# Performance work log

Hardware: AMD Instinct MI355X
Metric: run time of the kernel (lower is better)

Reference implementation:

```python
import jax, jax.numpy as jnp
import numpy as np

B, LQ, LA, H = 32, 1024, 1024, 512
NEG = -1e7


def setup_inputs() -> dict:
    key = jax.random.key(0)
    kq, ka, ku = jax.random.split(key, 3)
    q = jax.random.normal(kq, (B, LQ, H), dtype=jnp.float32)
    a = jax.random.normal(ka, (B, LA, H), dtype=jnp.float32)
    U = 0.02 * jax.random.normal(ku, (H, H), dtype=jnp.float32)  # init.normal(std=0.02)
    q_mask = jnp.ones((B, LQ, 1), dtype=jnp.float32)
    a_mask = jnp.ones((B, LA, 1), dtype=jnp.float32)
    return {"q": q, "a": a, "U": U, "q_mask": q_mask, "a_mask": a_mask}


def reference(q, a, U, q_mask, a_mask):
    # mask[b,i,j] = q_mask[b,i] * a_mask[b,j]  (nonzero => valid)
    mask = jnp.matmul(q_mask, jnp.swapaxes(a_mask, 1, 2)) > 0  # [B,LQ,LA] bool
    # bilinear score X = q @ U @ a^T
    qU = jnp.einsum('bqh,hk->bqk', q, U)
    X = jnp.einsum('bqk,bak->bqa', qU, a)  # [B,LQ,LA]
    X = jnp.where(mask, X, NEG)
    I = jax.nn.sigmoid(X)
    att_a2q = jnp.max(jax.nn.softmax(I, axis=-1), axis=-1)  # [B,LQ]
    att_q2a = jnp.max(jax.nn.softmax(I, axis=-2), axis=-2)  # [B,LA]
    q_attn = jnp.einsum('blh,bl->bh', q, att_a2q)  # [B,H]
    a_attn = jnp.einsum('blh,bl->bh', a, att_q2a)  # [B,H]
    return q_attn, a_attn
```

## Files before the change

kernel.cpp:

```cpp
#include <hip/hip_runtime.h>

typedef __attribute__((ext_vector_type(8))) short bf16x8;
typedef __attribute__((ext_vector_type(4))) float f32x4;
typedef unsigned short u16;
typedef unsigned int u32;

#define NLOG2E -1.44269504088896f
#define LOG2E   1.44269504088896f

__device__ __forceinline__ float bf2f(u16 x) {
  union { u32 u; float f; } v; v.u = ((u32)x) << 16; return v.f;
}
__device__ __forceinline__ u16 f2b(float f) {
  union { float f; u32 u; } v; v.f = f;
  return (u16)((v.u + 0x7FFFu + ((v.u >> 16) & 1u)) >> 16);
}
__device__ __forceinline__ bool inputs_are_bf16(const void* qmask) {
  return *(const u32*)qmask == 0x3F803F80u;
}
__device__ __forceinline__ u32 fkey(float f) {
  u32 b = __float_as_uint(f);
  return (b >> 31) ? ~b : (b | 0x80000000u);
}
__device__ __forceinline__ float fkey_inv(u32 k) {
  u32 b = (k & 0x80000000u) ? (k ^ 0x80000000u) : ~k;
  return __uint_as_float(b);
}

__global__ __launch_bounds__(256) void prep_all(
    const void* __restrict__ q, const void* __restrict__ a,
    const void* __restrict__ U, const void* __restrict__ qmask,
    u16* __restrict__ qb, u16* __restrict__ ab, u16* __restrict__ Ut,
    u32* __restrict__ stats, float* __restrict__ out)
{
  const bool bf = inputs_are_bf16(qmask);
  const int t = threadIdx.x;
  __shared__ u16 tile[64][65];
  if (blockIdx.x < 8192) {
    const int idx = blockIdx.x * 256 + t;
    if (idx < 131072) stats[idx] = (idx < 65536) ? 0u : 0xFFFFFFFFu;
    if (idx < 32768) out[idx] = 0.f;
    const size_t base = (size_t)idx * 8;
    if (bf) {
      *(bf16x8*)&qb[base] = ((const bf16x8*)q)[idx];
      *(bf16x8*)&ab[base] = ((const bf16x8*)a)[idx];
    } else {
      const float4* qf = (const float4*)q;
      const float4* af = (const float4*)a;
      float4 x0 = qf[2 * idx], x1 = qf[2 * idx + 1];
      u16 o[8] = {f2b(x0.x), f2b(x0.y), f2b(x0.z), f2b(x0.w),
                  f2b(x1.x), f2b(x1.y), f2b(x1.z), f2b(x1.w)};
      *(bf16x8*)&qb[base] = *(bf16x8*)o;
      float4 y0 = af[2 * idx], y1 = af[2 * idx + 1];
      u16 p[8] = {f2b(y0.x), f2b(y0.y), f2b(y0.z), f2b(y0.w),
                  f2b(y1.x), f2b(y1.y), f2b(y1.z), f2b(y1.w)};
      *(bf16x8*)&ab[base] = *(bf16x8*)p;
    }
  } else {
    const int bb = blockIdx.x - 8192;
    const int bx = bb & 7, by = bb >> 3;
    #pragma unroll
    for (int i = 0; i < 16; i++) {
      int r = i * 4 + (t >> 6);
      int c = t & 63;
      size_t gi = (size_t)(by * 64 + r) * 512 + bx * 64 + c;
      tile[c][r] = bf ? ((const u16*)U)[gi] : f2b(((const float*)U)[gi]);
    }
    __syncthreads();
    #pragma unroll
    for (int i = 0; i < 16; i++) {
      int r = i * 4 + (t >> 6);
      int c = t & 63;
      Ut[(size_t)(bx * 64 + r) * 512 + by * 64 + c] = tile[r][c];
    }
  }
}

template<int EPI>
__global__ __launch_bounds__(256) void gemm_bt(
    const u16* __restrict__ A, const u16* __restrict__ B,
    u16* __restrict__ C, float scaleC,
    size_t strideA, size_t strideB,
    const void* __restrict__ q_mask, const void* __restrict__ a_mask,
    float* __restrict__ rowsumA, float* __restrict__ colsumA,
    u32* __restrict__ rowkeyA, u32* __restrict__ colkeyA)
{
  __shared__ __align__(16) char smem[37888];
  u16* As = (u16*)smem;
  u16* Bs = (u16*)(smem + 16384);
  u16* Ct = (u16*)smem;
  float* redS = (float*)smem;
  float* redM = (float*)(smem + 16896);
  float* qp = (float*)(smem + 36864);
  float* ap = (float*)(smem + 37376);

  int bx, by, bz;
  if (EPI) {
    const int id = blockIdx.x;
    bz = id >> 6;
    const int w = id & 63;
    bx = w >> 3;
    by = ((w & 7) - bz) & 7;
  } else {
    bx = blockIdx.x; by = blockIdx.y; bz = blockIdx.z;
  }

  const int tid  = threadIdx.x;
  const int lane = tid & 63;
  const int wave = tid >> 6;
  const int wr = wave >> 1, wc = wave & 1;
  const int l15 = lane & 15, lq = lane >> 4;
  const int rsub = lane >> 3;
  const int csw  = (lane & 7) ^ rsub;

  const u16* Ab = A + strideA * bz + (size_t)by * 128 * 512;
  const u16* Bb = B + strideB * bz + (size_t)bx * 128 * 512;

  if (EPI) {
    const bool bf = inputs_are_bf16(q_mask);
    if (tid < 128) {
      int gi = bz * 1024 + by * 128 + tid;
      float v = bf ? bf2f(((const u16*)q_mask)[gi]) : ((const float*)q_mask)[gi];
      qp[tid] = (v > 0.f) ? 0.f : 1e30f;
    } else {
      int gj = bz * 1024 + bx * 128 + (tid - 128);
      float v = bf ? bf2f(((const u16*)a_mask)[gj]) : ((const float*)a_mask)[gj];
      ap[tid - 128] = (v > 0.f) ? 0.f : 1e30f;
    }
    __syncthreads();
  }

  f32x4 acc[4][4];
  if (EPI) {
    #pragma unroll
    for (int mt = 0; mt < 4; mt++)
      #pragma unroll
      for (int nt = 0; nt < 4; nt++) {
        float cp = ap[wc * 64 + nt * 16 + l15];
        #pragma unroll
        for (int r = 0; r < 4; r++)
          acc[mt][nt][r] = qp[wr * 64 + mt * 16 + lq * 4 + r] + cp;
      }
  } else {
    #pragma unroll
    for (int i = 0; i < 4; i++)
      #pragma unroll
      for (int j = 0; j < 4; j++) {
        f32x4 z = {0.f, 0.f, 0.f, 0.f};
        acc[i][j] = z;
      }
  }

  for (int k0 = 0; k0 < 512; k0 += 64) {
    #pragma unroll
    for (int i = 0; i < 4; i++) {
      const int r0 = wave * 32 + i * 8;
      const size_t go = (size_t)(r0 + rsub) * 512 + k0 + csw * 8;
      __builtin_amdgcn_global_load_lds(
          (const __attribute__((address_space(1))) void*)(Ab + go),
          (__attribute__((address_space(3))) void*)&As[r0 * 64], 16, 0, 0);
      __builtin_amdgcn_global_load_lds(
          (const __attribute__((address_space(1))) void*)(Bb + go),
          (__attribute__((address_space(3))) void*)&Bs[r0 * 64], 16, 0, 0);
    }
    __syncthreads();
    #pragma unroll
    for (int ks = 0; ks < 64; ks += 32) {
      const int cx = ((ks >> 3) + lq) ^ (l15 & 7);
      bf16x8 af[4], bfr[4];
      #pragma unroll
      for (int tt = 0; tt < 4; tt++) {
        af[tt]  = *(const bf16x8*)&As[(wr * 64 + tt * 16 + l15) * 64 + cx * 8];
        bfr[tt] = *(const bf16x8*)&Bs[(wc * 64 + tt * 16 + l15) * 64 + cx * 8];
      }
      #pragma unroll
      for (int mt = 0; mt < 4; mt++)
        #pragma unroll
        for (int nt = 0; nt < 4; nt++)
          acc[mt][nt] = __builtin_amdgcn_mfma_f32_16x16x32_bf16(af[mt], bfr[nt], acc[mt][nt], 0, 0, 0);
    }
    __syncthreads();
  }

  if (!EPI) {
    #pragma unroll
    for (int mt = 0; mt < 4; mt++)
      #pragma unroll
      for (int nt = 0; nt < 4; nt++)
        #pragma unroll
        for (int r = 0; r < 4; r++) {
          int row = wr * 64 + mt * 16 + lq * 4 + r;
          int col = wc * 64 + nt * 16 + l15;
          Ct[row * 144 + col] = f2b(scaleC * acc[mt][nt][r]);
        }
    __syncthreads();
    u16* Cb = C + (size_t)by * 128 * 512 + bx * 128;
    #pragma unroll
    for (int i = 0; i < 8; i++) {
      int c = tid + i * 256;
      int row = c >> 4, cc = c & 15;
      *(bf16x8*)&Cb[(size_t)row * 512 + cc * 8] = *(const bf16x8*)&Ct[row * 144 + cc * 8];
    }
  } else {
    const int gi0 = bz * 1024 + by * 128;
    const int gj0 = bz * 1024 + bx * 128;
    float csum[4] = {0.f, 0.f, 0.f, 0.f};
    float cmin[4] = {3e38f, 3e38f, 3e38f, 3e38f};
    #pragma unroll
    for (int mt = 0; mt < 4; mt++) {
      #pragma unroll
      for (int r = 0; r < 4; r++) {
        const int row = wr * 64 + mt * 16 + lq * 4 + r;
        float rsm = 0.f, rmn = 3e38f;
        #pragma unroll
        for (int nt = 0; nt < 4; nt++) {
          float y = acc[mt][nt][r];
          float u = __builtin_amdgcn_exp2f(y);
          float s = __builtin_amdgcn_rcpf(1.f + u);
          float e = __builtin_amdgcn_exp2f(LOG2E * s);
          rsm += e;
          csum[nt] += e;
          rmn = fminf(rmn, y);
          cmin[nt] = fminf(cmin[nt], y);
        }
        redS[row * 33 + l15 + 16 * wc] = rsm;
        redM[row * 33 + l15 + 16 * wc] = rmn;
      }
    }
    #pragma unroll
    for (int nt = 0; nt < 4; nt++) {
      float cs = csum[nt], cm = cmin[nt];
      cs += __shfl_xor(cs, 16); cm = fminf(cm, __shfl_xor(cm, 16));
      cs += __shfl_xor(cs, 32); cm = fminf(cm, __shfl_xor(cm, 32));
      if (lane < 16) {
        int gj = gj0 + wc * 64 + nt * 16 + l15;
        atomicAdd(&colsumA[gj], cs);
        atomicMin(&colkeyA[gj], fkey(cm));
      }
    }
    __syncthreads();
    if (tid < 128) {
      float s = 0.f;
      #pragma unroll
      for (int j = 0; j < 32; j++) s += redS[tid * 33 + j];
      atomicAdd(&rowsumA[gi0 + tid], s);
    } else {
      const int row = tid - 128;
      float m = 3e38f;
      #pragma unroll
      for (int j = 0; j < 32; j++) m = fminf(m, redM[row * 33 + j]);
      atomicMin(&rowkeyA[gi0 + row], fkey(m));
    }
  }
}

__global__ __launch_bounds__(256) void partial_kernel(
    const u16* __restrict__ qb, const u16* __restrict__ ab,
    const u32* __restrict__ stats, float* __restrict__ out)
{
  __shared__ float att[128];
  const int tid = threadIdx.x;
  const int hc = blockIdx.x, seg = blockIdx.y;
  const int b = blockIdx.z >> 1, half = blockIdx.z & 1;
  const float* sm = (const float*)stats + half * 32768 + b * 1024 + seg * 128;
  const u32* ky = stats + 65536 + half * 32768 + b * 1024 + seg * 128;
  if (tid < 128) {
    float ymin = fkey_inv(ky[tid]);
    float Imax = __builtin_amdgcn_rcpf(1.f + __builtin_amdgcn_exp2f(ymin));
    att[tid] = __expf(Imax) * __builtin_amdgcn_rcpf(sm[tid]);
  }
  __syncthreads();
  const u16* src = (half ? ab : qb) + (size_t)b * 524288 + (size_t)seg * 128 * 512;
  const int h = hc * 256 + tid;
  float acc = 0.f;
  #pragma unroll 8
  for (int i = 0; i < 128; i++) acc += bf2f(src[(size_t)i * 512 + h]) * att[i];
  atomicAdd(&out[half * 16384 + b * 512 + h], acc);
}

extern "C" void kernel_launch(void* const* d_in, const int* in_sizes, int n_in,
                              void* d_out, int out_size, void* d_ws, size_t ws_size,
                              hipStream_t stream) {
  const void* q  = d_in[0];
  const void* a  = d_in[1];
  const void* U  = d_in[2];
  const void* qm = d_in[3];
  const void* am = d_in[4];
  float* out = (float*)d_out;

  char* ws = (char*)d_ws;
  u16* qb    = (u16*)ws;
  u16* ab    = (u16*)(ws + 33554432);
  u16* qU    = (u16*)(ws + 67108864);
  u16* Ut    = (u16*)(ws + 100663296);
  u32* stats = (u32*)(ws + 101187584);
  float* rowsumA = (float*)stats;
  float* colsumA = (float*)stats + 32768;
  u32* rowkeyA = stats + 65536;
  u32* colkeyA = stats + 98304;

  prep_all<<<dim3(8256), dim3(256), 0, stream>>>(q, a, U, qm, qb, ab, Ut, stats, out);
  gemm_bt<0><<<dim3(4, 256, 1), dim3(256), 0, stream>>>(
      qb, Ut, qU, NLOG2E, (size_t)0, (size_t)0, qm, am,
      rowsumA, colsumA, rowkeyA, colkeyA);
  gemm_bt<1><<<dim3(2048), dim3(256), 0, stream>>>(
      qU, ab, (u16*)nullptr, 1.f, (size_t)524288, (size_t)524288, qm, am,
      rowsumA, colsumA, rowkeyA, colkeyA);
  partial_kernel<<<dim3(2, 8, 64), dim3(256), 0, stream>>>(qb, ab, stats, out);
}
```

Measured before the change: 257.9 us.

## Double-buffer GEMM LDS staging and replace stat atomics with per-slice partials

Both GEMM kernels now prefetch the next K-tile into a second LDS buffer while computing the current one. They use explicit vmcnt waits and barriers instead of two __syncthreads per iteration, and declare launch bounds for two blocks per CU. The score GEMM no longer does float atomicAdd and key-encoded atomicMin into global row and column stats. It writes per-tile partial sums and minima into slices, and partial_kernel reduces them, which also removes the stats init from prep_all. The costs are a larger LDS footprint, a plain 3D grid instead of the old swizzled block order, and reuse of the Ut workspace region for the partials once the first GEMM has finished.

```diff
diff --git a/kernel.cpp b/kernel.cpp
--- a/kernel.cpp
+++ b/kernel.cpp
@@ -7,6 +7,7 @@
 
 #define NLOG2E -1.44269504088896f
 #define LOG2E   1.44269504088896f
+#define SLICE 32768
 
 __device__ __forceinline__ float bf2f(u16 x) {
   union { u32 u; float f; } v; v.u = ((u32)x) << 16; return v.f;
@@ -17,28 +18,19 @@
 }
 __device__ __forceinline__ bool inputs_are_bf16(const void* qmask) {
   return *(const u32*)qmask == 0x3F803F80u;
-}
-__device__ __forceinline__ u32 fkey(float f) {
-  u32 b = __float_as_uint(f);
-  return (b >> 31) ? ~b : (b | 0x80000000u);
-}
-__device__ __forceinline__ float fkey_inv(u32 k) {
-  u32 b = (k & 0x80000000u) ? (k ^ 0x80000000u) : ~k;
-  return __uint_as_float(b);
 }
 
 __global__ __launch_bounds__(256) void prep_all(
     const void* __restrict__ q, const void* __restrict__ a,
     const void* __restrict__ U, const void* __restrict__ qmask,
     u16* __restrict__ qb, u16* __restrict__ ab, u16* __restrict__ Ut,
-    u32* __restrict__ stats, float* __restrict__ out)
+    float* __restrict__ out)
 {
   const bool bf = inputs_are_bf16(qmask);
   const int t = threadIdx.x;
   __shared__ u16 tile[64][65];
   if (blockIdx.x < 8192) {
     const int idx = blockIdx.x * 256 + t;
-    if (idx < 131072) stats[idx] = (idx < 65536) ? 0u : 0xFFFFFFFFu;
     if (idx < 32768) out[idx] = 0.f;
     const size_t base = (size_t)idx * 8;
     if (bf) {
@@ -77,34 +69,27 @@
 }
 
 template<int EPI>
-__global__ __launch_bounds__(256) void gemm_bt(
+__global__ __launch_bounds__(256, 2) void gemm_bt(
     const u16* __restrict__ A, const u16* __restrict__ B,
     u16* __restrict__ C, float scaleC,
     size_t strideA, size_t strideB,
     const void* __restrict__ q_mask, const void* __restrict__ a_mask,
-    float* __restrict__ rowsumA, float* __restrict__ colsumA,
-    u32* __restrict__ rowkeyA, u32* __restrict__ colkeyA)
+    float* __restrict__ statsP)
 {
-  __shared__ __align__(16) char smem[37888];
-  u16* As = (u16*)smem;
-  u16* Bs = (u16*)(smem + 16384);
-  u16* Ct = (u16*)smem;
+  __shared__ __align__(16) char smem[66560];
+  u16* As0 = (u16*)smem;
+  u16* Bs0 = (u16*)(smem + 16384);
+  u16* As1 = (u16*)(smem + 32768);
+  u16* Bs1 = (u16*)(smem + 49152);
+  u16* Ct  = (u16*)smem;
   float* redS = (float*)smem;
   float* redM = (float*)(smem + 16896);
-  float* qp = (float*)(smem + 36864);
-  float* ap = (float*)(smem + 37376);
-
-  int bx, by, bz;
-  if (EPI) {
-    const int id = blockIdx.x;
-    bz = id >> 6;
-    const int w = id & 63;
-    bx = w >> 3;
-    by = ((w & 7) - bz) & 7;
-  } else {
-    bx = blockIdx.x; by = blockIdx.y; bz = blockIdx.z;
-  }
-
+  float* colS = (float*)(smem + 33792);
+  float* colM = (float*)(smem + 34816);
+  float* qp = (float*)(smem + 65536);
+  float* ap = (float*)(smem + 66048);
+
+  const int bx = blockIdx.x, by = blockIdx.y, bz = blockIdx.z;
   const int tid  = threadIdx.x;
   const int lane = tid & 63;
   const int wave = tid >> 6;
@@ -151,27 +136,39 @@
       }
   }
 
-  for (int k0 = 0; k0 < 512; k0 += 64) {
+  auto stage = [&](u16* Asb, u16* Bsb, int k0) {
     #pragma unroll
     for (int i = 0; i < 4; i++) {
       const int r0 = wave * 32 + i * 8;
       const size_t go = (size_t)(r0 + rsub) * 512 + k0 + csw * 8;
       __builtin_amdgcn_global_load_lds(
           (const __attribute__((address_space(1))) void*)(Ab + go),
-          (__attribute__((address_space(3))) void*)&As[r0 * 64], 16, 0, 0);
+          (__attribute__((address_space(3))) void*)&Asb[r0 * 64], 16, 0, 0);
       __builtin_amdgcn_global_load_lds(
           (const __attribute__((address_space(1))) void*)(Bb + go),
-          (__attribute__((address_space(3))) void*)&Bs[r0 * 64], 16, 0, 0);
-    }
-    __syncthreads();
+          (__attribute__((address_space(3))) void*)&Bsb[r0 * 64], 16, 0, 0);
+    }
+  };
+
+  stage(As0, Bs0, 0);
+  #pragma unroll
+  for (int t = 0; t < 8; t++) {
+    u16* Asc = (t & 1) ? As1 : As0;
+    u16* Bsc = (t & 1) ? Bs1 : Bs0;
+    if (t < 7) {
+      stage((t & 1) ? As0 : As1, (t & 1) ? Bs0 : Bs1, (t + 1) * 64);
+      asm volatile("s_waitcnt vmcnt(8)\n\ts_barrier" ::: "memory");
+    } else {
+      asm volatile("s_waitcnt vmcnt(0)\n\ts_barrier" ::: "memory");
+    }
     #pragma unroll
     for (int ks = 0; ks < 64; ks += 32) {
       const int cx = ((ks >> 3) + lq) ^ (l15 & 7);
       bf16x8 af[4], bfr[4];
       #pragma unroll
       for (int tt = 0; tt < 4; tt++) {
-        af[tt]  = *(const bf16x8*)&As[(wr * 64 + tt * 16 + l15) * 64 + cx * 8];
-        bfr[tt] = *(const bf16x8*)&Bs[(wc * 64 + tt * 16 + l15) * 64 + cx * 8];
+        af[tt]  = *(const bf16x8*)&Asc[(wr * 64 + tt * 16 + l15) * 64 + cx * 8];
+        bfr[tt] = *(const bf16x8*)&Bsc[(wc * 64 + tt * 16 + l15) * 64 + cx * 8];
       }
       #pragma unroll
       for (int mt = 0; mt < 4; mt++)
@@ -179,7 +176,7 @@
         for (int nt = 0; nt < 4; nt++)
           acc[mt][nt] = __builtin_amdgcn_mfma_f32_16x16x32_bf16(af[mt], bfr[nt], acc[mt][nt], 0, 0, 0);
     }
-    __syncthreads();
+    asm volatile("s_waitcnt lgkmcnt(0)\n\ts_barrier" ::: "memory");
   }
 
   if (!EPI) {
@@ -204,6 +201,11 @@
   } else {
     const int gi0 = bz * 1024 + by * 128;
     const int gj0 = bz * 1024 + bx * 128;
+    float* rowsumP = statsP + 0      + bx * SLICE;
+    float* colsumP = statsP + 262144 + by * SLICE;
+    float* rowminP = statsP + 524288 + bx * SLICE;
+    float* colminP = statsP + 786432 + by * SLICE;
+
     float csum[4] = {0.f, 0.f, 0.f, 0.f};
     float cmin[4] = {3e38f, 3e38f, 3e38f, 3e38f};
     #pragma unroll
@@ -233,9 +235,9 @@
       cs += __shfl_xor(cs, 16); cm = fminf(cm, __shfl_xor(cm, 16));
       cs += __shfl_xor(cs, 32); cm = fminf(cm, __shfl_xor(cm, 32));
       if (lane < 16) {
-        int gj = gj0 + wc * 64 + nt * 16 + l15;
-        atomicAdd(&colsumA[gj], cs);
-        atomicMin(&colkeyA[gj], fkey(cm));
+        int j = wc * 64 + nt * 16 + l15;
+        colS[j * 2 + wr] = cs;
+        colM[j * 2 + wr] = cm;
       }
     }
     __syncthreads();
@@ -243,31 +245,39 @@
       float s = 0.f;
       #pragma unroll
       for (int j = 0; j < 32; j++) s += redS[tid * 33 + j];
-      atomicAdd(&rowsumA[gi0 + tid], s);
+      rowsumP[gi0 + tid] = s;
+      colsumP[gj0 + tid] = colS[tid * 2] + colS[tid * 2 + 1];
     } else {
-      const int row = tid - 128;
+      const int r = tid - 128;
       float m = 3e38f;
       #pragma unroll
-      for (int j = 0; j < 32; j++) m = fminf(m, redM[row * 33 + j]);
-      atomicMin(&rowkeyA[gi0 + row], fkey(m));
+      for (int j = 0; j < 32; j++) m = fminf(m, redM[r * 33 + j]);
+      rowminP[gi0 + r] = m;
+      colminP[gj0 + r] = fminf(colM[r * 2], colM[r * 2 + 1]);
     }
   }
 }
 
 __global__ __launch_bounds__(256) void partial_kernel(
     const u16* __restrict__ qb, const u16* __restrict__ ab,
-    const u32* __restrict__ stats, float* __restrict__ out)
+    const float* __restrict__ statsP, float* __restrict__ out)
 {
   __shared__ float att[128];
   const int tid = threadIdx.x;
   const int hc = blockIdx.x, seg = blockIdx.y;
   const int b = blockIdx.z >> 1, half = blockIdx.z & 1;
-  const float* sm = (const float*)stats + half * 32768 + b * 1024 + seg * 128;
-  const u32* ky = stats + 65536 + half * 32768 + b * 1024 + seg * 128;
   if (tid < 128) {
-    float ymin = fkey_inv(ky[tid]);
-    float Imax = __builtin_amdgcn_rcpf(1.f + __builtin_amdgcn_exp2f(ymin));
-    att[tid] = __expf(Imax) * __builtin_amdgcn_rcpf(sm[tid]);
+    const int g = b * 1024 + seg * 128 + tid;
+    const float* sumP = statsP + half * 262144;
+    const float* minP = statsP + 524288 + half * 262144;
+    float s = 0.f, m = 3e38f;
+    #pragma unroll
+    for (int s8 = 0; s8 < 8; s8++) {
+      s += sumP[s8 * SLICE + g];
+      m = fminf(m, minP[s8 * SLICE + g]);
+    }
+    float Imax = __builtin_amdgcn_rcpf(1.f + __builtin_amdgcn_exp2f(m));
+    att[tid] = __expf(Imax) * __builtin_amdgcn_rcpf(s);
   }
   __syncthreads();
   const u16* src = (half ? ab : qb) + (size_t)b * 524288 + (size_t)seg * 128 * 512;
@@ -293,18 +303,12 @@
   u16* ab    = (u16*)(ws + 33554432);
   u16* qU    = (u16*)(ws + 67108864);
   u16* Ut    = (u16*)(ws + 100663296);
-  u32* stats = (u32*)(ws + 101187584);
-  float* rowsumA = (float*)stats;
-  float* colsumA = (float*)stats + 32768;
-  u32* rowkeyA = stats + 65536;
-  u32* colkeyA = stats + 98304;
-
-  prep_all<<<dim3(8256), dim3(256), 0, stream>>>(q, a, U, qm, qb, ab, Ut, stats, out);
+  float* statsP = (float*)(ws + 100663296);
+
+  prep_all<<<dim3(8256), dim3(256), 0, stream>>>(q, a, U, qm, qb, ab, Ut, out);
   gemm_bt<0><<<dim3(4, 256, 1), dim3(256), 0, stream>>>(
-      qb, Ut, qU, NLOG2E, (size_t)0, (size_t)0, qm, am,
-      rowsumA, colsumA, rowkeyA, colkeyA);
-  gemm_bt<1><<<dim3(2048), dim3(256), 0, stream>>>(
-      qU, ab, (u16*)nullptr, 1.f, (size_t)524288, (size_t)524288, qm, am,
-      rowsumA, colsumA, rowkeyA, colkeyA);
-  partial_kernel<<<dim3(2, 8, 64), dim3(256), 0, stream>>>(qb, ab, stats, out);
-}
+      qb, Ut, qU, NLOG2E, (size_t)0, (size_t)0, qm, am, statsP);
+  gemm_bt<1><<<dim3(8, 8, 32), dim3(256), 0, stream>>>(
+      qU, ab, (u16*)nullptr, 1.f, (size_t)524288, (size_t)524288, qm, am, statsP);
+  partial_kernel<<<dim3(2, 8, 64), dim3(256), 0, stream>>>(qb, ab, statsP, out);
+}
```

New measurement: 250.9 us. 1.03x faster.
